# Optimization experiments

Measured on AMD Instinct MI355X. Metric: run time of the kernel, lower is better.

The kernel has to match this reference:

```python
import jax, jax.numpy as jnp
import numpy as np

N_DEC = 24        # num_hidden_layers * 2
IN_DIM = 768
HID = 128
OUT_DIM = 768 * 64 * 2 + 768 + 64  # 99136
BATCH = 64
GAIN = 1e-07


def _xavier(key, shape, gain):
    fan_in, fan_out = shape[-2], shape[-1]
    limit = gain * np.sqrt(6.0 / (fan_in + fan_out))
    return jax.random.uniform(key, shape, jnp.float32, -limit, limit)


def setup_inputs() -> dict:
    key = jax.random.key(0)
    k0, k1, k2 = jax.random.split(key, 3)
    x = jax.random.normal(k0, (BATCH, IN_DIM), jnp.float32)
    # stacked per-decoder weights (original: nn.ModuleList of N_DEC 2-layer MLPs)
    w1 = _xavier(k1, (N_DEC, IN_DIM, HID), GAIN)
    b1 = jnp.zeros((N_DEC, HID), jnp.float32)
    w2 = _xavier(k2, (N_DEC, HID, OUT_DIM), GAIN)
    b2 = jnp.zeros((N_DEC, OUT_DIM), jnp.float32)
    return {"hidden_inputs": x, "w1": w1, "b1": b1, "w2": w2, "b2": b2}


def reference(hidden_inputs, w1, b1, w2, b2):
    # Batched equivalent of the Python loop over N_DEC SimpleGenerators.
    # h: [n, b, hid]
    h = jax.nn.relu(jnp.einsum('bi,nih->nbh', hidden_inputs, w1) + b1[:, None, :])
    # out: [n, b, out_dim]  (original returns list of n arrays of shape [b, out_dim])
    out = jnp.einsum('nbh,nho->nbo', h, w2) + b2[:, None, :]
    return out
```

## Files before the change

### kernel.cpp

```cpp
#include <hip/hip_runtime.h>
#include <hip/hip_bf16.h>

#define N_DEC  24
#define IN_DIM 768
#define HID    128
#define ODIM   99136
#define BATCH  64
#define OTILE  256
#define NXBLK  ((ODIM + OTILE - 1) / OTILE)

typedef __attribute__((ext_vector_type(8))) short bf16x8;
typedef __attribute__((ext_vector_type(4))) float f32x4;

static __device__ __forceinline__ short f2bf_bits(float f) {
    union { __hip_bfloat16 b; short s; } u;
    u.b = __float2bfloat16(f);
    return u.s;
}

static __device__ __forceinline__ void gload_lds16(const float* src, float* dst) {
    __builtin_amdgcn_global_load_lds(
        (const __attribute__((address_space(1))) void*)src,
        (__attribute__((address_space(3))) void*)dst, 16, 0, 0);
}

__global__ __launch_bounds__(128) void gen_h_kernel(
    const float* __restrict__ x, const float* __restrict__ w1,
    const float* __restrict__ b1, __hip_bfloat16* __restrict__ hswz)
{
    const int nb = blockIdx.x;
    const int n  = nb >> 6;
    const int b  = nb & 63;
    const int t  = threadIdx.x;

    __shared__ float xs[IN_DIM];
    #pragma unroll
    for (int i = 0; i < IN_DIM / 128; ++i)
        xs[t + i * 128] = x[b * IN_DIM + t + i * 128];
    __syncthreads();

    const float* w = w1 + (size_t)n * IN_DIM * HID + t;
    float a0 = 0.f, a1 = 0.f, a2 = 0.f, a3 = 0.f;
    #pragma unroll 4
    for (int i = 0; i < IN_DIM; i += 4) {
        a0 = fmaf(xs[i + 0], w[(size_t)(i + 0) * HID], a0);
        a1 = fmaf(xs[i + 1], w[(size_t)(i + 1) * HID], a1);
        a2 = fmaf(xs[i + 2], w[(size_t)(i + 2) * HID], a2);
        a3 = fmaf(xs[i + 3], w[(size_t)(i + 3) * HID], a3);
    }
    float acc = (a0 + a1) + (a2 + a3) + b1[n * HID + t];
    acc = fmaxf(acc, 0.f);

    const int mt = b >> 4, lr = b & 15;
    const int ks = t >> 5, lg = (t >> 3) & 3, ii = t & 7;
    const size_t idx = (size_t)n * 8192
                     + (size_t)(((ks * 4 + mt) * 64) + lg * 16 + lr) * 8 + ii;
    hswz[idx] = __float2bfloat16(acc);
}

__global__ __launch_bounds__(256, 2) void gen_out_mfma(
    const __hip_bfloat16* __restrict__ hswz, const float* __restrict__ w2,
    const float* __restrict__ b2, float* __restrict__ out)
{
    const int n    = blockIdx.y;
    const int tid  = threadIdx.x;
    const int wave = tid >> 6;
    const int lane = tid & 63;
    const int lr   = lane & 15;
    const int lg   = lane >> 4;
    const long oblk = (long)blockIdx.x * OTILE;
    const long wcol = oblk + wave * 64;

    __shared__ float lds[2][4][32][64];

    const float* w2n = w2 + (size_t)n * HID * ODIM;

    auto stage = [&](int buf, int ks) {
        #pragma unroll
        for (int p = 0; p < 8; ++p) {
            const int r   = 4 * p + lg;
            const int swz = ((r >> 3) & 3) << 3;
            const long col = wcol + ((lr * 4) ^ swz);
            long c = col > (long)ODIM - 4 ? (long)ODIM - 4 : col;
            gload_lds16(w2n + (size_t)(ks * 32 + r) * ODIM + c,
                        &lds[buf][wave][4 * p][0]);
        }
    };

    stage(0, 0);

    const bf16x8* ha = (const bf16x8*)hswz + (size_t)n * 1024 + lane;
    bf16x8 a[4][4];
    #pragma unroll
    for (int mt = 0; mt < 4; ++mt)
        #pragma unroll
        for (int ks = 0; ks < 4; ++ks)
            a[mt][ks] = ha[(ks * 4 + mt) * 64];

    f32x4 bias4;
    const long ocol = wcol + lr * 4;
    {
        long c = ocol > (long)ODIM - 4 ? (long)ODIM - 4 : ocol;
        bias4 = *(const f32x4*)(b2 + (size_t)n * ODIM + c);
    }

    f32x4 acc[4][4];
    #pragma unroll
    for (int tt = 0; tt < 4; ++tt)
        #pragma unroll
        for (int mt = 0; mt < 4; ++mt)
            acc[tt][mt] = f32x4{0.f, 0.f, 0.f, 0.f};

    #pragma unroll
    for (int ks = 0; ks < 4; ++ks) {
        if (ks < 3) {
            stage((ks + 1) & 1, ks + 1);
            asm volatile("s_waitcnt vmcnt(8)" ::: "memory");
        } else {
            asm volatile("s_waitcnt vmcnt(0)" ::: "memory");
        }
        __builtin_amdgcn_sched_barrier(0);

        const int buf = ks & 1;
        #pragma unroll
        for (int tt = 0; tt < 4; ++tt) {
            const int csw = (tt * 16 + lr) ^ (lg << 3);
            const float* lp = &lds[buf][wave][lg * 8][csw];
            float bv[8];
            #pragma unroll
            for (int i = 0; i < 8; ++i)
                bv[i] = lp[(size_t)i * 64];
            bf16x8 bf;
            #pragma unroll
            for (int i = 0; i < 8; ++i)
                bf[i] = f2bf_bits(bv[i]);
            #pragma unroll
            for (int mt = 0; mt < 4; ++mt)
                acc[tt][mt] = __builtin_amdgcn_mfma_f32_16x16x32_bf16(
                                  a[mt][ks], bf, acc[tt][mt], 0, 0, 0);
        }
    }

    float* tb = &lds[0][wave][0][0];
    float* ob = out + ((size_t)n * BATCH) * ODIM;
    const int rr = lane >> 4;

    #pragma unroll
    for (int mt = 0; mt < 4; ++mt) {
        #pragma unroll
        for (int tt = 0; tt < 4; ++tt)
            #pragma unroll
            for (int r = 0; r < 4; ++r)
                tb[(lg * 4 + r) * 64 + ((tt * 16 + lr) ^ (lg << 3))] = acc[tt][mt][r];
        #pragma unroll
        for (int j = 0; j < 4; ++j) {
            f32x4 v = *(const f32x4*)&tb[(j * 4 + rr) * 64 + ((lr * 4) ^ ((j & 3) << 3))];
            v += bias4;
            if (ocol <= (long)ODIM - 4)
                *(f32x4*)(ob + (size_t)(mt * 16 + j * 4 + rr) * ODIM + ocol) = v;
        }
    }
}

extern "C" void kernel_launch(void* const* d_in, const int* in_sizes, int n_in,
                              void* d_out, int out_size, void* d_ws, size_t ws_size,
                              hipStream_t stream)
{
    const float* x  = (const float*)d_in[0];
    const float* w1 = (const float*)d_in[1];
    const float* b1 = (const float*)d_in[2];
    const float* w2 = (const float*)d_in[3];
    const float* b2 = (const float*)d_in[4];
    float* out = (float*)d_out;
    __hip_bfloat16* hbf = (__hip_bfloat16*)d_ws;

    gen_h_kernel<<<dim3(N_DEC * BATCH), dim3(128), 0, stream>>>(x, w1, b1, hbf);

    gen_out_mfma<<<dim3(NXBLK, N_DEC), dim3(256), 0, stream>>>(hbf, w2, b2, out);
}
```

Before: 372.8 us.

## Stage output tile block-wide in LDS and write full rows with nontemporal stores

The epilogue now transposes the whole 64x256 output tile through shared LDS, with bias added per column before the write, instead of a per-wave 64-column transpose. Each wave then writes 16 full rows of 256 contiguous floats, so each store instruction covers a 1 KB contiguous segment rather than 256-byte pieces. The stores use nontemporal hints to avoid polluting cache with the large streamed output. It adds two block-wide barriers and an extra sched_barrier, and it changes the bias load to scalar per-column loads.

```diff
diff --git a/kernel.cpp b/kernel.cpp
--- a/kernel.cpp
+++ b/kernel.cpp
@@ -97,11 +97,12 @@
         for (int ks = 0; ks < 4; ++ks)
             a[mt][ks] = ha[(ks * 4 + mt) * 64];
 
-    f32x4 bias4;
-    const long ocol = wcol + lr * 4;
-    {
-        long c = ocol > (long)ODIM - 4 ? (long)ODIM - 4 : ocol;
-        bias4 = *(const f32x4*)(b2 + (size_t)n * ODIM + c);
+    float bias_s[4];
+    #pragma unroll
+    for (int tt = 0; tt < 4; ++tt) {
+        long c = wcol + tt * 16 + lr;
+        if (c > (long)ODIM - 1) c = (long)ODIM - 1;
+        bias_s[tt] = b2[(size_t)n * ODIM + c];
     }
 
     f32x4 acc[4][4];
@@ -139,26 +140,34 @@
                 acc[tt][mt] = __builtin_amdgcn_mfma_f32_16x16x32_bf16(
                                   a[mt][ks], bf, acc[tt][mt], 0, 0, 0);
         }
+        __builtin_amdgcn_sched_barrier(0);
     }
 
-    float* tb = &lds[0][wave][0][0];
-    float* ob = out + ((size_t)n * BATCH) * ODIM;
-    const int rr = lane >> 4;
+    __syncthreads();
+    float* trs = &lds[0][0][0][0];
 
     #pragma unroll
-    for (int mt = 0; mt < 4; ++mt) {
+    for (int tt = 0; tt < 4; ++tt)
         #pragma unroll
-        for (int tt = 0; tt < 4; ++tt)
+        for (int mt = 0; mt < 4; ++mt)
             #pragma unroll
             for (int r = 0; r < 4; ++r)
-                tb[(lg * 4 + r) * 64 + ((tt * 16 + lr) ^ (lg << 3))] = acc[tt][mt][r];
-        #pragma unroll
-        for (int j = 0; j < 4; ++j) {
-            f32x4 v = *(const f32x4*)&tb[(j * 4 + rr) * 64 + ((lr * 4) ^ ((j & 3) << 3))];
-            v += bias4;
-            if (ocol <= (long)ODIM - 4)
-                *(f32x4*)(ob + (size_t)(mt * 16 + j * 4 + rr) * ODIM + ocol) = v;
-        }
+                trs[(mt * 16 + lg * 4 + r) * 256 +
+                    ((wave * 64 + tt * 16 + lr) ^ (lg << 3))] =
+                    acc[tt][mt][r] + bias_s[tt];
+
+    __syncthreads();
+
+    const long gc = oblk + lane * 4;
+    const bool ok = gc <= (long)ODIM - 4;
+    #pragma unroll
+    for (int j = 0; j < 16; ++j) {
+        const int R  = wave * 16 + j;
+        const int cR = ((j >> 2) & 3) << 3;
+        f32x4 v = *(const f32x4*)&trs[R * 256 + ((lane * 4) ^ cR)];
+        if (ok)
+            __builtin_nontemporal_store(
+                v, (f32x4*)(out + ((size_t)n * BATCH + R) * ODIM + gc));
     }
 }
 
```

New measurement: 369.5 us. About the same (-0.9%).
